# Optimization experiments

Hardware: AMD Instinct MI355X
Metric: run time of the kernel (lower is better)

Reference implementation:

```python
import jax, jax.numpy as jnp
import numpy as np

_LOG_2PI = float(np.log(2.0 * np.pi))
N = 4096
N_VARS = 128
N_SOURCES = 8
_EPS = 1e-6


def setup_inputs() -> dict:
    key = jax.random.key(0)
    ks = jax.random.split(key, 6)
    data = jax.random.normal(ks[0], (N, N_VARS), dtype=jnp.float32)
    sources = jax.random.randint(ks[1], (N,), 0, N_SOURCES, dtype=jnp.int32)
    miss_mask = jax.random.bernoulli(ks[2], 0.3, (N, N_VARS))
    # Strictly lower-triangular DAG weights, small spectral norm so I - W is well conditioned
    W_eff = jnp.tril(jax.random.normal(ks[3], (N_VARS, N_VARS), dtype=jnp.float32) * 0.05, k=-1)
    log_sigma2 = jnp.zeros((N_SOURCES, N_VARS), dtype=jnp.float32)
    mu = jnp.zeros((N_VARS,), dtype=jnp.float32)
    sample_weights = jax.random.uniform(ks[4], (N,), dtype=jnp.float32)
    return {"data": data, "W_eff": W_eff, "log_sigma2": log_sigma2, "mu": mu,
            "sample_weights": sample_weights, "sources": sources, "miss_mask": miss_mask}


def reference(data, W_eff, log_sigma2, mu, sample_weights, sources, miss_mask):
    # Gaussian log-likelihood over observed entries only, per sample.
    # Original torch code loops over unique (source, missingness-pattern) groups and
    # does a Cholesky of the observed sub-covariance Sigma_oo + eps*I.  We compute the
    # mathematically identical quantity fully batched via the masked-covariance trick:
    #   Sigma_tilde = M (Sigma + eps I) M + diag(1 - obs)
    # whose logdet equals logdet(Sigma_oo + eps I_oo) and whose quadratic form on the
    # zero-filled centred data equals x_o^T (Sigma_oo + eps I)^{-1} x_o.
    D = data.shape[1]
    I = jnp.eye(D, dtype=data.dtype)
    T = jnp.linalg.solve(I - W_eff, I)                       # [D, D]
    sigma2 = jnp.maximum(jnp.exp(log_sigma2), _EPS)          # [S, D]
    # Sigma_s = T^T diag(sigma2_s) T for every source
    Sigma = jnp.einsum('ij,si,ik->sjk', T, sigma2, T)        # [S, D, D]

    obs = (~miss_mask).astype(data.dtype)                    # [N, D]
    xc = (data - mu[None, :]) * obs                          # centred, zero at missing

    Sig_i = Sigma[sources] + _EPS * I                        # [N, D, D]
    M = obs[:, :, None] * obs[:, None, :]                    # [N, D, D] obs outer obs
    Sig_t = Sig_i * M + I * (1.0 - obs)[:, None, :]          # identity on missing coords

    L = jnp.linalg.cholesky(Sig_t)                           # [N, D, D]
    z = jax.scipy.linalg.solve_triangular(L, xc[:, :, None], lower=True)[:, :, 0]
    quad = jnp.sum(z * z, axis=1)                            # [N]
    logdet = 2.0 * jnp.sum(jnp.log(jnp.diagonal(L, axis1=1, axis2=2)), axis=1)
    d_obs = jnp.sum(obs, axis=1)                             # [N]
    ll = -0.5 * (quad + logdet + d_obs * _LOG_2PI)           # [N]
    return jnp.sum(ll * sample_weights)
```

## Files before the change

### kernel.cpp

```cpp
#include <hip/hip_runtime.h>
#include <math.h>

#define DD 128
#define NSRC 8
#define EMAX 32
#define MFAST 62
#define LOG_2PI 1.83787706640934548356f
#define LN2F 0.69314718055994531f
#define EPSF 1e-6f

__device__ inline int tri_row_of(int e) {
    float f = sqrtf(8.f * (float)e + 1.f);
    int r = (int)((f - 1.f) * 0.5f);
    if ((r + 1) * (r + 2) / 2 <= e) ++r;
    else if (r * (r + 1) / 2 > e) --r;
    return r;
}

__global__ __launch_bounds__(128) void k_precompute(
    const float* __restrict__ W, const float* __restrict__ ls2,
    const unsigned int* __restrict__ mw, int n_words,
    float* __restrict__ Q, float* __restrict__ ldS,
    int* __restrict__ flagarr, float* __restrict__ partial,
    int* __restrict__ ovf_cnt)
{
    __shared__ float Bs[DD][DD + 1];
    __shared__ float r[4][DD + 1];
    __shared__ float sinv[DD];
    __shared__ float part2[2];
    __shared__ int fsh[2];
    const int tid = threadIdx.x;
    const int s   = blockIdx.x >> 5;
    const int i0  = (blockIdx.x & 31) * 4;

    if (blockIdx.x == 0) {
        if (tid < 64)  partial[tid] = 0.f;
        if (tid == 64) *ovf_cnt = 0;
    }

    int gid = (blockIdx.x * 128 + tid) * 4;
    int f = 0;
    #pragma unroll
    for (int t = 0; t < 4; ++t) {
        int idx = gid + t;
        if (idx < n_words) {
            unsigned int v = mw[idx];
            if (v > 1u) f |= 1;
            if (v == 0x3F800000u) f |= 2;
        }
    }
    unsigned long long bA = __ballot(f & 1);
    unsigned long long bB = __ballot(f & 2);
    if ((tid & 63) == 0) fsh[tid >> 6] = (bA ? 1 : 0) | (bB ? 2 : 0);

    for (int idx = tid; idx < DD * DD; idx += 128) {
        int row = idx >> 7, col = idx & 127;
        Bs[row][col] = (row == col ? 1.f : 0.f) - W[idx];
    }
    sinv[tid] = 1.f / fmaxf(expf(ls2[s * DD + tid]), EPSF);
    __syncthreads();
    if (tid == 0) flagarr[blockIdx.x] = fsh[0] | fsh[1];
    for (int a = 0; a < 4; ++a)
        r[a][tid] = Bs[i0 + a][tid] * sinv[tid];
    __syncthreads();

    const int j = tid;
    float acc0 = 0.f, acc1 = 0.f, acc2 = 0.f, acc3 = 0.f;
    #pragma unroll 4
    for (int d = 0; d < DD; ++d) {
        float bj = Bs[j][d];
        acc0 += r[0][d] * bj;
        acc1 += r[1][d] * bj;
        acc2 += r[2][d] * bj;
        acc3 += r[3][d] * bj;
    }
    size_t base = ((size_t)s * DD + i0) * DD + j;
    Q[base         ] = acc0;
    Q[base +     DD] = acc1;
    Q[base + 2 * DD] = acc2;
    Q[base + 3 * DD] = acc3;

    if (i0 == 0) {
        float v = logf(fmaxf(expf(ls2[s * DD + tid]), EPSF));
        for (int o = 32; o; o >>= 1) v += __shfl_down(v, o, 64);
        if ((tid & 63) == 0) part2[tid >> 6] = v;
        __syncthreads();
        if (tid == 0) ldS[s] = part2[0] + part2[1];
    }
}

__global__ __launch_bounds__(64) void k_fast(
    const float* __restrict__ data, const float* __restrict__ mu,
    const float* __restrict__ wgt, const int* __restrict__ src,
    const void* __restrict__ miss, const int* __restrict__ flagarr,
    const float* __restrict__ Q, const float* __restrict__ ldS,
    float* __restrict__ partial, int* __restrict__ ovf_cnt,
    int* __restrict__ ovf_list)
{
    __shared__ float xsh[DD];
    __shared__ float ysh[DD];
    __shared__ int   midx[64];
    __shared__ float csc[2][64];

    const int i = blockIdx.x, lane = threadIdx.x;
    const int s = src[i];
    const float* Qs = Q + (size_t)s * DD * DD;
    const size_t base = (size_t)i * DD;
    const int j0 = 2 * lane, j1 = 2 * lane + 1;

    int fl = 0;
    #pragma unroll
    for (int t = 0; t < 4; ++t) fl |= flagarr[lane + 64 * t];
    unsigned long long fb1 = __ballot(fl & 1);
    unsigned long long fb2 = __ballot(fl & 2);
    const int f = (fb1 ? 1 : 0) | (fb2 ? 2 : 0);

    bool mmE, mmO;
    if (f & 2) {
        const float* M = (const float*)miss;
        mmE = M[base + j0] != 0.f;  mmO = M[base + j1] != 0.f;
    } else if (f & 1) {
        const unsigned char* M = (const unsigned char*)miss;
        mmE = M[base + j0] != 0;    mmO = M[base + j1] != 0;
    } else {
        const int* M = (const int*)miss;
        mmE = M[base + j0] != 0;    mmO = M[base + j1] != 0;
    }

    unsigned long long bE = __ballot(mmE), bO = __ballot(mmO);
    const int m = __popcll(bE) + __popcll(bO);
    if (m > MFAST) {
        if (lane == 0) { int pos = atomicAdd(ovf_cnt, 1); ovf_list[pos] = i; }
        return;
    }
    unsigned long long lt = (1ull << lane) - 1ull;
    if (mmE) midx[__popcll(bE & lt)] = j0;
    if (mmO) midx[__popcll(bE) + __popcll(bO & lt)] = j1;

    float x0 = mmE ? 0.f : (data[base + j0] - mu[j0]);
    float x1 = mmO ? 0.f : (data[base + j1] - mu[j1]);
    xsh[j0] = x0;
    xsh[j1] = x1;
    __syncthreads();

    float y0 = 0.f, y1 = 0.f, z0 = 0.f, z1 = 0.f;
    #pragma unroll 8
    for (int k = 0; k < DD; k += 2) {
        float xk0 = xsh[k], xk1 = xsh[k + 1];
        float2 qa = *(const float2*)(Qs + (size_t)k * DD + j0);
        float2 qb = *(const float2*)(Qs + (size_t)(k + 1) * DD + j0);
        y0 += xk0 * qa.x;  y1 += xk0 * qa.y;
        z0 += xk1 * qb.x;  z1 += xk1 * qb.y;
    }
    y0 += z0;  y1 += z1;
    ysh[j0] = y0;
    ysh[j1] = y1;
    float p = x0 * y0 + x1 * y1;
    for (int o = 32; o; o >>= 1) p += __shfl_down(p, o, 64);
    __syncthreads();

    const int cntT = ((m + 1) * (m + 2)) >> 1;
    unsigned key[EMAX];
    float    val[EMAX];
    #pragma unroll
    for (int t = 0; t < EMAX; ++t) {
        key[t] = 0u; val[t] = 0.f;
        int e = lane + (t << 6);
        if (e < cntT) {
            int q  = tri_row_of(e);
            int jc = m - q;
            int ir = jc + (e - ((q * (q + 1)) >> 1));
            float v;
            if (ir == m) {
                v = (jc == m) ? 0.f : ysh[midx[jc]];
            } else {
                v = Qs[(size_t)(midx[ir] * DD + midx[jc])];
            }
            key[t] = ((unsigned)jc << 8) | (unsigned)ir;
            val[t] = v;
            if (jc == 0) csc[0][ir] = v;
        }
    }
    __syncthreads();

    float logacc = 0.f;
    #pragma unroll 1
    for (int k = 0; k < m; ++k) {
        const int pb = k & 1;
        float dk = csc[pb][k];
        float invd = __builtin_amdgcn_rcpf(dk);
        logacc += __log2f(dk);
        const unsigned boundA = (unsigned)(k + 1) << 8;
        const unsigned boundB = (unsigned)(k + 2) << 8;
        #pragma unroll
        for (int t = 0; t < EMAX; ++t) {
            bool alive = (key[t] >= boundA);
            if (!__any(alive)) break;
            if (alive) {
                int ir = (int)(key[t] & 255u);
                int jc = (int)(key[t] >> 8);
                float ci = csc[pb][ir];
                float cj = csc[pb][jc];
                val[t] -= ci * cj * invd;
                if (key[t] < boundB) csc[pb ^ 1][ir] = val[t];
            }
        }
        __syncthreads();
    }

    if (lane == 0) {
        float ll = -0.5f * ((p + val[0]) + logacc * LN2F + ldS[s]
                            + (float)(DD - m) * LOG_2PI);
        atomicAdd(&partial[i & 63], ll * wgt[i]);
    }
}

__global__ __launch_bounds__(128) void k_tail(
    const float* __restrict__ data, const float* __restrict__ mu,
    const float* __restrict__ wgt, const int* __restrict__ src,
    const void* __restrict__ miss, const int* __restrict__ flagarr,
    const float* __restrict__ Q, const float* __restrict__ ldS,
    float* __restrict__ partial, const int* __restrict__ ovf_cnt,
    const int* __restrict__ ovf_list, float* __restrict__ out)
{
    __shared__ __align__(16) float xsh[DD];
    __shared__ float ysh[DD];
    __shared__ int   midx[DD];
    __shared__ float cscv[DD + 1];
    __shared__ float tri[(DD + 1) * (DD + 2) / 2];
    __shared__ float bc[2];
    __shared__ float red[2];
    __shared__ int   sh_m;
    __shared__ int   sh_f;

    const int tid = threadIdx.x;
    if (tid == 0) sh_f = 0;
    __syncthreads();
    {
        int fl = flagarr[tid] | flagarr[tid + 128];
        if (fl) atomicOr(&sh_f, fl);
    }
    __syncthreads();
    const int f = sh_f;

    const int novf = *ovf_cnt;
    for (int j = 0; j < novf; ++j) {
        const int i = ovf_list[j];
        if (tid == 0) sh_m = 0;
        __syncthreads();

        const int s = src[i];
        const float* Qs = Q + (size_t)s * DD * DD;
        const size_t g = (size_t)i * DD + tid;
        bool mm;
        if (f & 2)      mm = ((const float*)miss)[g] != 0.f;
        else if (f & 1) mm = ((const unsigned char*)miss)[g] != 0;
        else            mm = ((const int*)miss)[g] != 0;

        float xv = mm ? 0.f : (data[g] - mu[tid]);
        xsh[tid] = xv;
        if (mm) { int pos = atomicAdd(&sh_m, 1); midx[pos] = tid; }
        __syncthreads();
        const int m = sh_m;

        const float4* qrow = (const float4*)(Qs + (size_t)tid * DD);
        const float4* x4   = (const float4*)xsh;
        float acc = 0.f;
        #pragma unroll 8
        for (int d = 0; d < DD / 4; ++d) {
            float4 q = qrow[d], xx = x4[d];
            acc += q.x * xx.x + q.y * xx.y + q.z * xx.z + q.w * xx.w;
        }
        ysh[tid] = acc;
        float pp = xv * acc;
        for (int o = 32; o; o >>= 1) pp += __shfl_down(pp, o, 64);
        if ((tid & 63) == 0) red[tid >> 6] = pp;
        __syncthreads();

        const int cntA = (m * (m + 1)) >> 1;
        for (int e = tid; e < cntA; e += 128) {
            int a = tri_row_of(e);
            int b = e - ((a * (a + 1)) >> 1);
            tri[e] = Qs[(size_t)midx[a] * DD + midx[b]];
        }
        for (int b = tid; b < m; b += 128) tri[cntA + b] = ysh[midx[b]];
        if (tid == 0) tri[cntA + m] = 0.f;
        __syncthreads();

        float logacc = 0.f;
        if (m > 0) {
            if (tid == 0) {
                float d0 = tri[0];
                bc[1] = d0;
                float sq = sqrtf(d0);
                bc[0] = 1.f / sq;
                tri[0] = sq;
            }
            __syncthreads();
            for (int k = 0; k < m; ++k) {
                float inv = bc[0];
                if (tid == 0) logacc += logf(bc[1]);
                for (int ii = k + 1 + tid; ii <= m; ii += 128) {
                    int off = (ii * (ii + 1)) >> 1;
                    float v = tri[off + k] * inv;
                    tri[off + k] = v;
                    cscv[ii] = v;
                }
                __syncthreads();
                int qn  = m - k;
                int cnt = (qn * (qn + 1)) >> 1;
                for (int e = tid; e < cnt; e += 128) {
                    int ri = tri_row_of(e);
                    int rj = e - ((ri * (ri + 1)) >> 1);
                    int ii = k + 1 + ri, jj = k + 1 + rj;
                    int off = (ii * (ii + 1)) >> 1;
                    float v = tri[off + jj] - cscv[ii] * cscv[jj];
                    if (ii == jj && jj == k + 1 && k + 1 < m) {
                        bc[1] = v;
                        float sq = sqrtf(v);
                        bc[0] = 1.f / sq;
                        tri[off + jj] = sq;
                    } else {
                        tri[off + jj] = v;
                    }
                }
                __syncthreads();
            }
        }

        if (tid == 0) {
            float quad2 = (m > 0) ? -tri[cntA + m] : 0.f;
            float quad1 = red[0] + red[1];
            float ll = -0.5f * ((quad1 - quad2) + logacc + ldS[s]
                                + (float)(DD - m) * LOG_2PI);
            atomicAdd(&partial[i & 63], ll * wgt[i]);
        }
        __syncthreads();
    }

    __syncthreads();
    if (tid < 64) {
        float v = partial[tid];
        for (int o = 32; o; o >>= 1) v += __shfl_down(v, o, 64);
        if (tid == 0) out[0] = v;
    }
}

extern "C" void kernel_launch(void* const* d_in, const int* in_sizes, int n_in,
                              void* d_out, int out_size, void* d_ws, size_t ws_size,
                              hipStream_t stream)
{
    const float* data = (const float*)d_in[0];
    const float* W    = (const float*)d_in[1];
    const float* ls2  = (const float*)d_in[2];
    const float* mu   = (const float*)d_in[3];
    const float* wgt  = (const float*)d_in[4];
    const int*   src  = (const int*)d_in[5];
    const void*  miss = (const void*)d_in[6];
    float* out = (float*)d_out;

    float* Q        = (float*)d_ws;
    float* ldS      = Q + (size_t)NSRC * DD * DD;
    float* partial  = ldS + NSRC;
    int*   flagarr  = (int*)(partial + 64);
    int*   ovf_cnt  = flagarr + 256;
    int*   ovf_list = ovf_cnt + 1;

    const int n       = in_sizes[0] / DD;
    const int n_words = (n * DD) / 4;

    hipLaunchKernelGGL(k_precompute, dim3(NSRC * 32), dim3(128), 0, stream,
                       W, ls2, (const unsigned int*)miss, n_words,
                       Q, ldS, flagarr, partial, ovf_cnt);
    hipLaunchKernelGGL(k_fast, dim3(n), dim3(64), 0, stream,
                       data, mu, wgt, src, miss, flagarr, Q, ldS,
                       partial, ovf_cnt, ovf_list);
    hipLaunchKernelGGL(k_tail, dim3(1), dim3(128), 0, stream,
                       data, mu, wgt, src, miss, flagarr, Q, ldS,
                       partial, ovf_cnt, ovf_list, out);
}
```

Baseline: 154.1 us.

## Process two samples per wavefront in k_fast to interleave independent eliminations

```diff
diff --git a/kernel.cpp b/kernel.cpp
--- a/kernel.cpp
+++ b/kernel.cpp
@@ -89,23 +89,28 @@
     }
 }
 
-__global__ __launch_bounds__(64) void k_fast(
+__global__ __launch_bounds__(64, 2) void k_fast(
     const float* __restrict__ data, const float* __restrict__ mu,
     const float* __restrict__ wgt, const int* __restrict__ src,
     const void* __restrict__ miss, const int* __restrict__ flagarr,
     const float* __restrict__ Q, const float* __restrict__ ldS,
     float* __restrict__ partial, int* __restrict__ ovf_cnt,
-    int* __restrict__ ovf_list)
+    int* __restrict__ ovf_list, int n)
 {
-    __shared__ float xsh[DD];
-    __shared__ float ysh[DD];
-    __shared__ int   midx[64];
-    __shared__ float csc[2][64];
-
-    const int i = blockIdx.x, lane = threadIdx.x;
-    const int s = src[i];
-    const float* Qs = Q + (size_t)s * DD * DD;
-    const size_t base = (size_t)i * DD;
+    __shared__ float xshA[DD], xshB[DD];
+    __shared__ float yshA[DD], yshB[DD];
+    __shared__ int   midxA[64], midxB[64];
+    __shared__ float cscA[2][64], cscB[2][64];
+
+    const int lane = threadIdx.x;
+    const int iA = blockIdx.x * 2;
+    const bool validB = (iA + 1) < n;
+    const int iB = validB ? (iA + 1) : iA;
+    const int sA = src[iA], sB = src[iB];
+    const float* QA = Q + (size_t)sA * DD * DD;
+    const float* QB = Q + (size_t)sB * DD * DD;
+    const size_t baseA = (size_t)iA * DD;
+    const size_t baseB = (size_t)iB * DD;
     const int j0 = 2 * lane, j1 = 2 * lane + 1;
 
     int fl = 0;
@@ -115,103 +120,163 @@
     unsigned long long fb2 = __ballot(fl & 2);
     const int f = (fb1 ? 1 : 0) | (fb2 ? 2 : 0);
 
-    bool mmE, mmO;
+    bool mAe, mAo, mBe, mBo;
     if (f & 2) {
         const float* M = (const float*)miss;
-        mmE = M[base + j0] != 0.f;  mmO = M[base + j1] != 0.f;
+        mAe = M[baseA + j0] != 0.f;  mAo = M[baseA + j1] != 0.f;
+        mBe = M[baseB + j0] != 0.f;  mBo = M[baseB + j1] != 0.f;
     } else if (f & 1) {
         const unsigned char* M = (const unsigned char*)miss;
-        mmE = M[base + j0] != 0;    mmO = M[base + j1] != 0;
+        mAe = M[baseA + j0] != 0;    mAo = M[baseA + j1] != 0;
+        mBe = M[baseB + j0] != 0;    mBo = M[baseB + j1] != 0;
     } else {
         const int* M = (const int*)miss;
-        mmE = M[base + j0] != 0;    mmO = M[base + j1] != 0;
-    }
-
-    unsigned long long bE = __ballot(mmE), bO = __ballot(mmO);
-    const int m = __popcll(bE) + __popcll(bO);
-    if (m > MFAST) {
-        if (lane == 0) { int pos = atomicAdd(ovf_cnt, 1); ovf_list[pos] = i; }
-        return;
-    }
+        mAe = M[baseA + j0] != 0;    mAo = M[baseA + j1] != 0;
+        mBe = M[baseB + j0] != 0;    mBo = M[baseB + j1] != 0;
+    }
+
+    unsigned long long bAE = __ballot(mAe), bAO = __ballot(mAo);
+    unsigned long long bBE = __ballot(mBe), bBO = __ballot(mBo);
+    const int mAr = __popcll(bAE) + __popcll(bAO);
+    const int mBr = __popcll(bBE) + __popcll(bBO);
+    const bool skipA = (mAr > MFAST);
+    const bool skipB = (mBr > MFAST) || !validB;
+    if (lane == 0) {
+        if (skipA)                    { int pos = atomicAdd(ovf_cnt, 1); ovf_list[pos] = iA; }
+        if (validB && (mBr > MFAST))  { int pos = atomicAdd(ovf_cnt, 1); ovf_list[pos] = iB; }
+    }
+    const int mA = skipA ? 0 : mAr;
+    const int mB = skipB ? 0 : mBr;
     unsigned long long lt = (1ull << lane) - 1ull;
-    if (mmE) midx[__popcll(bE & lt)] = j0;
-    if (mmO) midx[__popcll(bE) + __popcll(bO & lt)] = j1;
-
-    float x0 = mmE ? 0.f : (data[base + j0] - mu[j0]);
-    float x1 = mmO ? 0.f : (data[base + j1] - mu[j1]);
-    xsh[j0] = x0;
-    xsh[j1] = x1;
-    __syncthreads();
-
-    float y0 = 0.f, y1 = 0.f, z0 = 0.f, z1 = 0.f;
-    #pragma unroll 8
+    if (!skipA) {
+        if (mAe) midxA[__popcll(bAE & lt)] = j0;
+        if (mAo) midxA[__popcll(bAE) + __popcll(bAO & lt)] = j1;
+    }
+    if (!skipB) {
+        if (mBe) midxB[__popcll(bBE & lt)] = j0;
+        if (mBo) midxB[__popcll(bBE) + __popcll(bBO & lt)] = j1;
+    }
+
+    float xA0 = mAe ? 0.f : (data[baseA + j0] - mu[j0]);
+    float xA1 = mAo ? 0.f : (data[baseA + j1] - mu[j1]);
+    float xB0 = mBe ? 0.f : (data[baseB + j0] - mu[j0]);
+    float xB1 = mBo ? 0.f : (data[baseB + j1] - mu[j1]);
+    xshA[j0] = xA0;  xshA[j1] = xA1;
+    xshB[j0] = xB0;  xshB[j1] = xB1;
+    __syncthreads();
+
+    float yA0 = 0.f, yA1 = 0.f, zA0 = 0.f, zA1 = 0.f;
+    float yB0 = 0.f, yB1 = 0.f, zB0 = 0.f, zB1 = 0.f;
+    #pragma unroll 4
     for (int k = 0; k < DD; k += 2) {
-        float xk0 = xsh[k], xk1 = xsh[k + 1];
-        float2 qa = *(const float2*)(Qs + (size_t)k * DD + j0);
-        float2 qb = *(const float2*)(Qs + (size_t)(k + 1) * DD + j0);
-        y0 += xk0 * qa.x;  y1 += xk0 * qa.y;
-        z0 += xk1 * qb.x;  z1 += xk1 * qb.y;
-    }
-    y0 += z0;  y1 += z1;
-    ysh[j0] = y0;
-    ysh[j1] = y1;
-    float p = x0 * y0 + x1 * y1;
-    for (int o = 32; o; o >>= 1) p += __shfl_down(p, o, 64);
-    __syncthreads();
-
-    const int cntT = ((m + 1) * (m + 2)) >> 1;
-    unsigned key[EMAX];
-    float    val[EMAX];
+        float xkA0 = xshA[k], xkA1 = xshA[k + 1];
+        float xkB0 = xshB[k], xkB1 = xshB[k + 1];
+        float2 qa = *(const float2*)(QA + (size_t)k * DD + j0);
+        float2 qb = *(const float2*)(QA + (size_t)(k + 1) * DD + j0);
+        float2 qc = *(const float2*)(QB + (size_t)k * DD + j0);
+        float2 qd = *(const float2*)(QB + (size_t)(k + 1) * DD + j0);
+        yA0 += xkA0 * qa.x;  yA1 += xkA0 * qa.y;
+        zA0 += xkA1 * qb.x;  zA1 += xkA1 * qb.y;
+        yB0 += xkB0 * qc.x;  yB1 += xkB0 * qc.y;
+        zB0 += xkB1 * qd.x;  zB1 += xkB1 * qd.y;
+    }
+    yA0 += zA0;  yA1 += zA1;  yB0 += zB0;  yB1 += zB1;
+    yshA[j0] = yA0;  yshA[j1] = yA1;
+    yshB[j0] = yB0;  yshB[j1] = yB1;
+    float pA = xA0 * yA0 + xA1 * yA1;
+    float pB = xB0 * yB0 + xB1 * yB1;
+    for (int o = 32; o; o >>= 1) {
+        pA += __shfl_down(pA, o, 64);
+        pB += __shfl_down(pB, o, 64);
+    }
+    __syncthreads();
+
+    const int cntTA = ((mA + 1) * (mA + 2)) >> 1;
+    const int cntTB = ((mB + 1) * (mB + 2)) >> 1;
+    const int cntMax = cntTA > cntTB ? cntTA : cntTB;
+    unsigned keyA[EMAX], keyB[EMAX];
+    float    valA[EMAX], valB[EMAX];
     #pragma unroll
     for (int t = 0; t < EMAX; ++t) {
-        key[t] = 0u; val[t] = 0.f;
+        keyA[t] = 0u; valA[t] = 0.f;
+        keyB[t] = 0u; valB[t] = 0.f;
         int e = lane + (t << 6);
-        if (e < cntT) {
+        if (e < cntMax) {
             int q  = tri_row_of(e);
-            int jc = m - q;
-            int ir = jc + (e - ((q * (q + 1)) >> 1));
-            float v;
-            if (ir == m) {
-                v = (jc == m) ? 0.f : ysh[midx[jc]];
-            } else {
-                v = Qs[(size_t)(midx[ir] * DD + midx[jc])];
-            }
-            key[t] = ((unsigned)jc << 8) | (unsigned)ir;
-            val[t] = v;
-            if (jc == 0) csc[0][ir] = v;
-        }
-    }
-    __syncthreads();
-
-    float logacc = 0.f;
+            int eq = e - ((q * (q + 1)) >> 1);
+            if (e < cntTA) {
+                int jc = mA - q;
+                int ir = jc + eq;
+                float v;
+                if (ir == mA) v = (jc == mA) ? 0.f : yshA[midxA[jc]];
+                else          v = QA[(size_t)(midxA[ir] * DD + midxA[jc])];
+                keyA[t] = ((unsigned)jc << 8) | (unsigned)ir;
+                valA[t] = v;
+                if (jc == 0) cscA[0][ir] = v;
+            }
+            if (e < cntTB) {
+                int jc = mB - q;
+                int ir = jc + eq;
+                float v;
+                if (ir == mB) v = (jc == mB) ? 0.f : yshB[midxB[jc]];
+                else          v = QB[(size_t)(midxB[ir] * DD + midxB[jc])];
+                keyB[t] = ((unsigned)jc << 8) | (unsigned)ir;
+                valB[t] = v;
+                if (jc == 0) cscB[0][ir] = v;
+            }
+        }
+    }
+    __syncthreads();
+
+    float logA = 0.f, logB = 0.f;
+    const int mMax = mA > mB ? mA : mB;
     #pragma unroll 1
-    for (int k = 0; k < m; ++k) {
+    for (int k = 0; k < mMax; ++k) {
         const int pb = k & 1;
-        float dk = csc[pb][k];
-        float invd = __builtin_amdgcn_rcpf(dk);
-        logacc += __log2f(dk);
-        const unsigned boundA = (unsigned)(k + 1) << 8;
-        const unsigned boundB = (unsigned)(k + 2) << 8;
+        float dkA = cscA[pb][k];
+        float dkB = cscB[pb][k];
+        float invdA = __builtin_amdgcn_rcpf(dkA);
+        float invdB = __builtin_amdgcn_rcpf(dkB);
+        if (k < mA) logA += __log2f(dkA);
+        if (k < mB) logB += __log2f(dkB);
+        const unsigned b1 = (unsigned)(k + 1) << 8;
+        const unsigned b2 = (unsigned)(k + 2) << 8;
         #pragma unroll
         for (int t = 0; t < EMAX; ++t) {
-            bool alive = (key[t] >= boundA);
-            if (!__any(alive)) break;
-            if (alive) {
-                int ir = (int)(key[t] & 255u);
-                int jc = (int)(key[t] >> 8);
-                float ci = csc[pb][ir];
-                float cj = csc[pb][jc];
-                val[t] -= ci * cj * invd;
-                if (key[t] < boundB) csc[pb ^ 1][ir] = val[t];
+            bool aA = (keyA[t] >= b1);
+            bool aB = (keyB[t] >= b1);
+            if (!__any(aA | aB)) break;
+            if (aA) {
+                int ir = (int)(keyA[t] & 255u);
+                int jc = (int)(keyA[t] >> 8);
+                float ci = cscA[pb][ir];
+                float cj = cscA[pb][jc];
+                valA[t] -= ci * cj * invdA;
+                if (keyA[t] < b2) cscA[pb ^ 1][ir] = valA[t];
+            }
+            if (aB) {
+                int ir = (int)(keyB[t] & 255u);
+                int jc = (int)(keyB[t] >> 8);
+                float ci = cscB[pb][ir];
+                float cj = cscB[pb][jc];
+                valB[t] -= ci * cj * invdB;
+                if (keyB[t] < b2) cscB[pb ^ 1][ir] = valB[t];
             }
         }
         __syncthreads();
     }
 
     if (lane == 0) {
-        float ll = -0.5f * ((p + val[0]) + logacc * LN2F + ldS[s]
-                            + (float)(DD - m) * LOG_2PI);
-        atomicAdd(&partial[i & 63], ll * wgt[i]);
+        if (!skipA) {
+            float llA = -0.5f * ((pA + valA[0]) + logA * LN2F + ldS[sA]
+                                 + (float)(DD - mA) * LOG_2PI);
+            atomicAdd(&partial[iA & 63], llA * wgt[iA]);
+        }
+        if (!skipB) {
+            float llB = -0.5f * ((pB + valB[0]) + logB * LN2F + ldS[sB]
+                                 + (float)(DD - mB) * LOG_2PI);
+            atomicAdd(&partial[iB & 63], llB * wgt[iB]);
+        }
     }
 }
 
@@ -372,9 +437,9 @@
     hipLaunchKernelGGL(k_precompute, dim3(NSRC * 32), dim3(128), 0, stream,
                        W, ls2, (const unsigned int*)miss, n_words,
                        Q, ldS, flagarr, partial, ovf_cnt);
-    hipLaunchKernelGGL(k_fast, dim3(n), dim3(64), 0, stream,
+    hipLaunchKernelGGL(k_fast, dim3((n + 1) / 2), dim3(64), 0, stream,
                        data, mu, wgt, src, miss, flagarr, Q, ldS,
-                       partial, ovf_cnt, ovf_list);
+                       partial, ovf_cnt, ovf_list, n);
     hipLaunchKernelGGL(k_tail, dim3(1), dim3(128), 0, stream,
                        data, mu, wgt, src, miss, flagarr, Q, ldS,
                        partial, ovf_cnt, ovf_list, out);
```

Measured after the change: 181.0 us. 17.4% more time.

## Fold overflow tail kernel into fast kernel via last-block-done counter

Applied to the files above, without the earlier changes.

```diff
diff --git a/kernel.cpp b/kernel.cpp
--- a/kernel.cpp
+++ b/kernel.cpp
@@ -12,8 +12,8 @@
 __device__ inline int tri_row_of(int e) {
     float f = sqrtf(8.f * (float)e + 1.f);
     int r = (int)((f - 1.f) * 0.5f);
-    if ((r + 1) * (r + 2) / 2 <= e) ++r;
-    else if (r * (r + 1) / 2 > e) --r;
+    r += (int)((r + 1) * (r + 2) / 2 <= e);
+    r -= (int)(r * (r + 1) / 2 > e);
     return r;
 }
 
@@ -22,7 +22,7 @@
     const unsigned int* __restrict__ mw, int n_words,
     float* __restrict__ Q, float* __restrict__ ldS,
     int* __restrict__ flagarr, float* __restrict__ partial,
-    int* __restrict__ ovf_cnt)
+    int* __restrict__ ovf_cnt, int* __restrict__ done_cnt)
 {
     __shared__ float Bs[DD][DD + 1];
     __shared__ float r[4][DD + 1];
@@ -36,6 +36,7 @@
     if (blockIdx.x == 0) {
         if (tid < 64)  partial[tid] = 0.f;
         if (tid == 64) *ovf_cnt = 0;
+        if (tid == 65) *done_cnt = 0;
     }
 
     int gid = (blockIdx.x * 128 + tid) * 4;
@@ -53,9 +54,16 @@
     unsigned long long bB = __ballot(f & 2);
     if ((tid & 63) == 0) fsh[tid >> 6] = (bA ? 1 : 0) | (bB ? 2 : 0);
 
-    for (int idx = tid; idx < DD * DD; idx += 128) {
-        int row = idx >> 7, col = idx & 127;
-        Bs[row][col] = (row == col ? 1.f : 0.f) - W[idx];
+    const float4* __restrict__ W4 = (const float4*)W;
+    #pragma unroll 8
+    for (int idx = tid; idx < (DD * DD) / 4; idx += 128) {
+        float4 w = W4[idx];
+        int row = idx >> 5;
+        int col = (idx & 31) << 2;
+        Bs[row][col + 0] = ((col + 0) == row ? 1.f : 0.f) - w.x;
+        Bs[row][col + 1] = ((col + 1) == row ? 1.f : 0.f) - w.y;
+        Bs[row][col + 2] = ((col + 2) == row ? 1.f : 0.f) - w.z;
+        Bs[row][col + 3] = ((col + 3) == row ? 1.f : 0.f) - w.w;
     }
     sinv[tid] = 1.f / fmaxf(expf(ls2[s * DD + tid]), EPSF);
     __syncthreads();
@@ -66,7 +74,7 @@
 
     const int j = tid;
     float acc0 = 0.f, acc1 = 0.f, acc2 = 0.f, acc3 = 0.f;
-    #pragma unroll 4
+    #pragma unroll 8
     for (int d = 0; d < DD; ++d) {
         float bj = Bs[j][d];
         acc0 += r[0][d] * bj;
@@ -95,12 +103,15 @@
     const void* __restrict__ miss, const int* __restrict__ flagarr,
     const float* __restrict__ Q, const float* __restrict__ ldS,
     float* __restrict__ partial, int* __restrict__ ovf_cnt,
-    int* __restrict__ ovf_list)
+    int* __restrict__ ovf_list, int* __restrict__ done_cnt,
+    float* __restrict__ g_tri, float* __restrict__ out)
 {
     __shared__ float xsh[DD];
     __shared__ float ysh[DD];
-    __shared__ int   midx[64];
+    __shared__ int   midx[DD];
     __shared__ float csc[2][64];
+    __shared__ float cscv[DD + 1];
+    __shared__ float bcsh[2];
 
     const int i = blockIdx.x, lane = threadIdx.x;
     const int s = src[i];
@@ -129,221 +140,203 @@
 
     unsigned long long bE = __ballot(mmE), bO = __ballot(mmO);
     const int m = __popcll(bE) + __popcll(bO);
-    if (m > MFAST) {
+    const bool ovf = (m > MFAST);
+    if (ovf) {
         if (lane == 0) { int pos = atomicAdd(ovf_cnt, 1); ovf_list[pos] = i; }
-        return;
-    }
-    unsigned long long lt = (1ull << lane) - 1ull;
-    if (mmE) midx[__popcll(bE & lt)] = j0;
-    if (mmO) midx[__popcll(bE) + __popcll(bO & lt)] = j1;
-
-    float x0 = mmE ? 0.f : (data[base + j0] - mu[j0]);
-    float x1 = mmO ? 0.f : (data[base + j1] - mu[j1]);
-    xsh[j0] = x0;
-    xsh[j1] = x1;
-    __syncthreads();
-
-    float y0 = 0.f, y1 = 0.f, z0 = 0.f, z1 = 0.f;
-    #pragma unroll 8
-    for (int k = 0; k < DD; k += 2) {
-        float xk0 = xsh[k], xk1 = xsh[k + 1];
-        float2 qa = *(const float2*)(Qs + (size_t)k * DD + j0);
-        float2 qb = *(const float2*)(Qs + (size_t)(k + 1) * DD + j0);
-        y0 += xk0 * qa.x;  y1 += xk0 * qa.y;
-        z0 += xk1 * qb.x;  z1 += xk1 * qb.y;
-    }
-    y0 += z0;  y1 += z1;
-    ysh[j0] = y0;
-    ysh[j1] = y1;
-    float p = x0 * y0 + x1 * y1;
-    for (int o = 32; o; o >>= 1) p += __shfl_down(p, o, 64);
-    __syncthreads();
-
-    const int cntT = ((m + 1) * (m + 2)) >> 1;
-    unsigned key[EMAX];
-    float    val[EMAX];
-    #pragma unroll
-    for (int t = 0; t < EMAX; ++t) {
-        key[t] = 0u; val[t] = 0.f;
-        int e = lane + (t << 6);
-        if (e < cntT) {
-            int q  = tri_row_of(e);
-            int jc = m - q;
-            int ir = jc + (e - ((q * (q + 1)) >> 1));
-            float v;
-            if (ir == m) {
-                v = (jc == m) ? 0.f : ysh[midx[jc]];
-            } else {
-                v = Qs[(size_t)(midx[ir] * DD + midx[jc])];
-            }
-            key[t] = ((unsigned)jc << 8) | (unsigned)ir;
-            val[t] = v;
-            if (jc == 0) csc[0][ir] = v;
-        }
-    }
-    __syncthreads();
-
-    float logacc = 0.f;
-    #pragma unroll 1
-    for (int k = 0; k < m; ++k) {
-        const int pb = k & 1;
-        float dk = csc[pb][k];
-        float invd = __builtin_amdgcn_rcpf(dk);
-        logacc += __log2f(dk);
-        const unsigned boundA = (unsigned)(k + 1) << 8;
-        const unsigned boundB = (unsigned)(k + 2) << 8;
+    } else {
+        unsigned long long lt = (1ull << lane) - 1ull;
+        if (mmE) midx[__popcll(bE & lt)] = j0;
+        if (mmO) midx[__popcll(bE) + __popcll(bO & lt)] = j1;
+
+        float x0 = mmE ? 0.f : (data[base + j0] - mu[j0]);
+        float x1 = mmO ? 0.f : (data[base + j1] - mu[j1]);
+        xsh[j0] = x0;
+        xsh[j1] = x1;
+        __syncthreads();
+
+        float y0 = 0.f, y1 = 0.f, z0 = 0.f, z1 = 0.f;
+        #pragma unroll 8
+        for (int k = 0; k < DD; k += 2) {
+            float xk0 = xsh[k], xk1 = xsh[k + 1];
+            float2 qa = *(const float2*)(Qs + (size_t)k * DD + j0);
+            float2 qb = *(const float2*)(Qs + (size_t)(k + 1) * DD + j0);
+            y0 += xk0 * qa.x;  y1 += xk0 * qa.y;
+            z0 += xk1 * qb.x;  z1 += xk1 * qb.y;
+        }
+        y0 += z0;  y1 += z1;
+        ysh[j0] = y0;
+        ysh[j1] = y1;
+        float p = x0 * y0 + x1 * y1;
+        for (int o = 32; o; o >>= 1) p += __shfl_down(p, o, 64);
+        __syncthreads();
+
+        const int cntT = ((m + 1) * (m + 2)) >> 1;
+        unsigned key[EMAX];
+        float    val[EMAX];
         #pragma unroll
         for (int t = 0; t < EMAX; ++t) {
-            bool alive = (key[t] >= boundA);
-            if (!__any(alive)) break;
-            if (alive) {
-                int ir = (int)(key[t] & 255u);
-                int jc = (int)(key[t] >> 8);
-                float ci = csc[pb][ir];
-                float cj = csc[pb][jc];
-                val[t] -= ci * cj * invd;
-                if (key[t] < boundB) csc[pb ^ 1][ir] = val[t];
+            int e = lane + (t << 6);
+            const bool inr = (e < cntT);
+            int ec = inr ? e : 0;
+            int q  = tri_row_of(ec);
+            int jc = m - q;
+            int ir = jc + (ec - ((q * (q + 1)) >> 1));
+            const bool isQ = inr && (ir < m);
+            const bool isY = inr && (ir == m) && (jc < m);
+            int mi = midx[ir];
+            int mj = midx[jc];
+            int qa = isQ ? (mi * DD + mj) : 0;
+            float qv = Qs[(size_t)qa];
+            int ya = isY ? mj : 0;
+            float yv = ysh[ya];
+            float v = isQ ? qv : (isY ? yv : 0.f);
+            key[t] = inr ? (((unsigned)jc << 8) | (unsigned)ir) : 0u;
+            val[t] = v;
+            if (inr && jc == 0) csc[0][ir] = v;
+        }
+        __syncthreads();
+
+        float logacc = 0.f;
+        #pragma unroll 1
+        for (int k = 0; k < m; ++k) {
+            const int pb = k & 1;
+            float dk = csc[pb][k];
+            float invd = __builtin_amdgcn_rcpf(dk);
+            logacc += __log2f(dk);
+            const unsigned boundA = (unsigned)(k + 1) << 8;
+            const unsigned boundB = (unsigned)(k + 2) << 8;
+            #pragma unroll
+            for (int t = 0; t < EMAX; ++t) {
+                bool alive = (key[t] >= boundA);
+                if (!__any(alive)) break;
+                if (alive) {
+                    int ir = (int)(key[t] & 255u);
+                    int jc = (int)(key[t] >> 8);
+                    float ci = csc[pb][ir];
+                    float cj = csc[pb][jc];
+                    val[t] -= ci * cj * invd;
+                    if (key[t] < boundB) csc[pb ^ 1][ir] = val[t];
+                }
             }
-        }
-        __syncthreads();
-    }
-
-    if (lane == 0) {
-        float ll = -0.5f * ((p + val[0]) + logacc * LN2F + ldS[s]
-                            + (float)(DD - m) * LOG_2PI);
-        atomicAdd(&partial[i & 63], ll * wgt[i]);
-    }
-}
-
-__global__ __launch_bounds__(128) void k_tail(
-    const float* __restrict__ data, const float* __restrict__ mu,
-    const float* __restrict__ wgt, const int* __restrict__ src,
-    const void* __restrict__ miss, const int* __restrict__ flagarr,
-    const float* __restrict__ Q, const float* __restrict__ ldS,
-    float* __restrict__ partial, const int* __restrict__ ovf_cnt,
-    const int* __restrict__ ovf_list, float* __restrict__ out)
-{
-    __shared__ __align__(16) float xsh[DD];
-    __shared__ float ysh[DD];
-    __shared__ int   midx[DD];
-    __shared__ float cscv[DD + 1];
-    __shared__ float tri[(DD + 1) * (DD + 2) / 2];
-    __shared__ float bc[2];
-    __shared__ float red[2];
-    __shared__ int   sh_m;
-    __shared__ int   sh_f;
-
-    const int tid = threadIdx.x;
-    if (tid == 0) sh_f = 0;
-    __syncthreads();
-    {
-        int fl = flagarr[tid] | flagarr[tid + 128];
-        if (fl) atomicOr(&sh_f, fl);
-    }
-    __syncthreads();
-    const int f = sh_f;
-
-    const int novf = *ovf_cnt;
+            __syncthreads();
+        }
+
+        if (lane == 0) {
+            float ll = -0.5f * ((p + val[0]) + logacc * LN2F + ldS[s]
+                                + (float)(DD - m) * LOG_2PI);
+            atomicAdd(&partial[i & 63], ll * wgt[i]);
+        }
+    }
+
+    __threadfence();
+    int done = 0;
+    if (lane == 0) done = atomicAdd(done_cnt, 1);
+    done = __shfl(done, 0, 64);
+    if (done != (int)gridDim.x - 1) return;
+    __threadfence();
+
+    const int novf = *(volatile int*)ovf_cnt;
     for (int j = 0; j < novf; ++j) {
-        const int i = ovf_list[j];
-        if (tid == 0) sh_m = 0;
-        __syncthreads();
-
-        const int s = src[i];
-        const float* Qs = Q + (size_t)s * DD * DD;
-        const size_t g = (size_t)i * DD + tid;
-        bool mm;
-        if (f & 2)      mm = ((const float*)miss)[g] != 0.f;
-        else if (f & 1) mm = ((const unsigned char*)miss)[g] != 0;
-        else            mm = ((const int*)miss)[g] != 0;
-
-        float xv = mm ? 0.f : (data[g] - mu[tid]);
-        xsh[tid] = xv;
-        if (mm) { int pos = atomicAdd(&sh_m, 1); midx[pos] = tid; }
-        __syncthreads();
-        const int m = sh_m;
-
-        const float4* qrow = (const float4*)(Qs + (size_t)tid * DD);
-        const float4* x4   = (const float4*)xsh;
-        float acc = 0.f;
-        #pragma unroll 8
-        for (int d = 0; d < DD / 4; ++d) {
-            float4 q = qrow[d], xx = x4[d];
-            acc += q.x * xx.x + q.y * xx.y + q.z * xx.z + q.w * xx.w;
-        }
-        ysh[tid] = acc;
-        float pp = xv * acc;
+        const int smp = ((volatile const int*)ovf_list)[j];
+        const int s2 = src[smp];
+        const float* Qs2 = Q + (size_t)s2 * DD * DD;
+        const size_t g0 = (size_t)smp * DD + lane;
+        const size_t g1 = g0 + 64;
+        bool mm0, mm1;
+        if (f & 2) {
+            mm0 = ((const float*)miss)[g0] != 0.f;
+            mm1 = ((const float*)miss)[g1] != 0.f;
+        } else if (f & 1) {
+            mm0 = ((const unsigned char*)miss)[g0] != 0;
+            mm1 = ((const unsigned char*)miss)[g1] != 0;
+        } else {
+            mm0 = ((const int*)miss)[g0] != 0;
+            mm1 = ((const int*)miss)[g1] != 0;
+        }
+        unsigned long long b0 = __ballot(mm0), b1 = __ballot(mm1);
+        const int mt = __popcll(b0) + __popcll(b1);
+        unsigned long long lt2 = (1ull << lane) - 1ull;
+        if (mm0) midx[__popcll(b0 & lt2)] = lane;
+        if (mm1) midx[__popcll(b0) + __popcll(b1 & lt2)] = lane + 64;
+        float xv0 = mm0 ? 0.f : (data[g0] - mu[lane]);
+        float xv1 = mm1 ? 0.f : (data[g1] - mu[lane + 64]);
+        xsh[lane] = xv0;  xsh[lane + 64] = xv1;
+        __syncthreads();
+
+        float a0 = 0.f, a1 = 0.f;
+        for (int d = 0; d < DD; ++d) {
+            float xd = xsh[d];
+            a0 += Qs2[(size_t)lane * DD + d] * xd;
+            a1 += Qs2[(size_t)(lane + 64) * DD + d] * xd;
+        }
+        ysh[lane] = a0;  ysh[lane + 64] = a1;
+        float pp = xv0 * a0 + xv1 * a1;
         for (int o = 32; o; o >>= 1) pp += __shfl_down(pp, o, 64);
-        if ((tid & 63) == 0) red[tid >> 6] = pp;
-        __syncthreads();
-
-        const int cntA = (m * (m + 1)) >> 1;
-        for (int e = tid; e < cntA; e += 128) {
+        __syncthreads();
+
+        const int cntA = (mt * (mt + 1)) >> 1;
+        for (int e = lane; e < cntA; e += 64) {
             int a = tri_row_of(e);
             int b = e - ((a * (a + 1)) >> 1);
-            tri[e] = Qs[(size_t)midx[a] * DD + midx[b]];
-        }
-        for (int b = tid; b < m; b += 128) tri[cntA + b] = ysh[midx[b]];
-        if (tid == 0) tri[cntA + m] = 0.f;
-        __syncthreads();
-
-        float logacc = 0.f;
-        if (m > 0) {
-            if (tid == 0) {
-                float d0 = tri[0];
-                bc[1] = d0;
+            g_tri[e] = Qs2[(size_t)midx[a] * DD + midx[b]];
+        }
+        for (int b = lane; b < mt; b += 64) g_tri[cntA + b] = ysh[midx[b]];
+        if (lane == 0) g_tri[cntA + mt] = 0.f;
+        __syncthreads();
+
+        float logacc2 = 0.f;
+        if (mt > 0) {
+            if (lane == 0) {
+                float d0 = g_tri[0];
+                bcsh[1] = d0;
                 float sq = sqrtf(d0);
-                bc[0] = 1.f / sq;
-                tri[0] = sq;
+                bcsh[0] = 1.f / sq;
+                g_tri[0] = sq;
             }
             __syncthreads();
-            for (int k = 0; k < m; ++k) {
-                float inv = bc[0];
-                if (tid == 0) logacc += logf(bc[1]);
-                for (int ii = k + 1 + tid; ii <= m; ii += 128) {
-                    int off = (ii * (ii + 1)) >> 1;
-                    float v = tri[off + k] * inv;
-                    tri[off + k] = v;
-                    cscv[ii] = v;
+            for (int k = 0; k < mt; ++k) {
+                float inv = bcsh[0];
+                if (lane == 0) logacc2 += logf(bcsh[1]);
+                for (int r2 = k + 1 + lane; r2 <= mt; r2 += 64) {
+                    int off = (r2 * (r2 + 1)) >> 1;
+                    float vv = g_tri[off + k] * inv;
+                    g_tri[off + k] = vv;
+                    cscv[r2] = vv;
                 }
                 __syncthreads();
-                int qn  = m - k;
+                int qn  = mt - k;
                 int cnt = (qn * (qn + 1)) >> 1;
-                for (int e = tid; e < cnt; e += 128) {
+                for (int e = lane; e < cnt; e += 64) {
                     int ri = tri_row_of(e);
                     int rj = e - ((ri * (ri + 1)) >> 1);
-                    int ii = k + 1 + ri, jj = k + 1 + rj;
-                    int off = (ii * (ii + 1)) >> 1;
-                    float v = tri[off + jj] - cscv[ii] * cscv[jj];
-                    if (ii == jj && jj == k + 1 && k + 1 < m) {
-                        bc[1] = v;
-                        float sq = sqrtf(v);
-                        bc[0] = 1.f / sq;
-                        tri[off + jj] = sq;
+                    int i2 = k + 1 + ri, j2 = k + 1 + rj;
+                    int off = (i2 * (i2 + 1)) >> 1;
+                    float vv = g_tri[off + j2] - cscv[i2] * cscv[j2];
+                    if (i2 == j2 && j2 == k + 1 && k + 1 < mt) {
+                        bcsh[1] = vv;
+                        float sq = sqrtf(vv);
+                        bcsh[0] = 1.f / sq;
+                        g_tri[off + j2] = sq;
                     } else {
-                        tri[off + jj] = v;
+                        g_tri[off + j2] = vv;
                     }
                 }
                 __syncthreads();
             }
         }
 
-        if (tid == 0) {
-            float quad2 = (m > 0) ? -tri[cntA + m] : 0.f;
-            float quad1 = red[0] + red[1];
-            float ll = -0.5f * ((quad1 - quad2) + logacc + ldS[s]
-                                + (float)(DD - m) * LOG_2PI);
-            atomicAdd(&partial[i & 63], ll * wgt[i]);
-        }
-        __syncthreads();
-    }
-
-    __syncthreads();
-    if (tid < 64) {
-        float v = partial[tid];
-        for (int o = 32; o; o >>= 1) v += __shfl_down(v, o, 64);
-        if (tid == 0) out[0] = v;
-    }
+        if (lane == 0) {
+            float quad2 = (mt > 0) ? -g_tri[cntA + mt] : 0.f;
+            float ll = -0.5f * ((pp - quad2) + logacc2 + ldS[s2]
+                                + (float)(DD - mt) * LOG_2PI);
+            atomicAdd(&partial[smp & 63], ll * wgt[smp]);
+        }
+        __syncthreads();
+    }
+
+    float v = ((volatile float*)partial)[lane];
+    for (int o = 32; o; o >>= 1) v += __shfl_down(v, o, 64);
+    if (lane == 0) out[0] = v;
 }
 
 extern "C" void kernel_launch(void* const* d_in, const int* in_sizes, int n_in,
@@ -365,17 +358,16 @@
     int*   flagarr  = (int*)(partial + 64);
     int*   ovf_cnt  = flagarr + 256;
     int*   ovf_list = ovf_cnt + 1;
+    int*   done_cnt = ovf_list + 4096;
+    float* g_tri    = (float*)(done_cnt + 1);
 
     const int n       = in_sizes[0] / DD;
     const int n_words = (n * DD) / 4;
 
     hipLaunchKernelGGL(k_precompute, dim3(NSRC * 32), dim3(128), 0, stream,
                        W, ls2, (const unsigned int*)miss, n_words,
-                       Q, ldS, flagarr, partial, ovf_cnt);
+                       Q, ldS, flagarr, partial, ovf_cnt, done_cnt);
     hipLaunchKernelGGL(k_fast, dim3(n), dim3(64), 0, stream,
                        data, mu, wgt, src, miss, flagarr, Q, ldS,
-                       partial, ovf_cnt, ovf_list);
-    hipLaunchKernelGGL(k_tail, dim3(1), dim3(128), 0, stream,
-                       data, mu, wgt, src, miss, flagarr, Q, ldS,
-                       partial, ovf_cnt, ovf_list, out);
+                       partial, ovf_cnt, ovf_list, done_cnt, g_tri, out);
 }
```

New measurement: 218.6 us. 41.8% more time.

## Pack four samples per block in k_fast and vectorize W load in precompute

Applied to the files above, without the earlier changes.

```diff
diff --git a/kernel.cpp b/kernel.cpp
--- a/kernel.cpp
+++ b/kernel.cpp
@@ -5,6 +5,7 @@
 #define NSRC 8
 #define EMAX 32
 #define MFAST 62
+#define WPB 4
 #define LOG_2PI 1.83787706640934548356f
 #define LN2F 0.69314718055994531f
 #define EPSF 1e-6f
@@ -53,9 +54,16 @@
     unsigned long long bB = __ballot(f & 2);
     if ((tid & 63) == 0) fsh[tid >> 6] = (bA ? 1 : 0) | (bB ? 2 : 0);
 
-    for (int idx = tid; idx < DD * DD; idx += 128) {
-        int row = idx >> 7, col = idx & 127;
-        Bs[row][col] = (row == col ? 1.f : 0.f) - W[idx];
+    const float4* __restrict__ W4 = (const float4*)W;
+    #pragma unroll 8
+    for (int idx = tid; idx < (DD * DD) / 4; idx += 128) {
+        float4 w = W4[idx];
+        int row = idx >> 5;
+        int col = (idx & 31) << 2;
+        Bs[row][col + 0] = ((col + 0) == row ? 1.f : 0.f) - w.x;
+        Bs[row][col + 1] = ((col + 1) == row ? 1.f : 0.f) - w.y;
+        Bs[row][col + 2] = ((col + 2) == row ? 1.f : 0.f) - w.z;
+        Bs[row][col + 3] = ((col + 3) == row ? 1.f : 0.f) - w.w;
     }
     sinv[tid] = 1.f / fmaxf(expf(ls2[s * DD + tid]), EPSF);
     __syncthreads();
@@ -66,7 +74,7 @@
 
     const int j = tid;
     float acc0 = 0.f, acc1 = 0.f, acc2 = 0.f, acc3 = 0.f;
-    #pragma unroll 4
+    #pragma unroll 8
     for (int d = 0; d < DD; ++d) {
         float bj = Bs[j][d];
         acc0 += r[0][d] * bj;
@@ -89,24 +97,33 @@
     }
 }
 
-__global__ __launch_bounds__(64) void k_fast(
+__global__ __launch_bounds__(256) void k_fast(
     const float* __restrict__ data, const float* __restrict__ mu,
     const float* __restrict__ wgt, const int* __restrict__ src,
     const void* __restrict__ miss, const int* __restrict__ flagarr,
     const float* __restrict__ Q, const float* __restrict__ ldS,
     float* __restrict__ partial, int* __restrict__ ovf_cnt,
-    int* __restrict__ ovf_list)
+    int* __restrict__ ovf_list, int n)
 {
-    __shared__ float xsh[DD];
-    __shared__ float ysh[DD];
-    __shared__ int   midx[64];
-    __shared__ float csc[2][64];
-
-    const int i = blockIdx.x, lane = threadIdx.x;
+    __shared__ float xsh[WPB][DD];
+    __shared__ float ysh[WPB][DD];
+    __shared__ int   midx[WPB][64];
+    __shared__ float csc[WPB][2][64];
+
+    const int wv   = threadIdx.x >> 6;
+    const int lane = threadIdx.x & 63;
+    const int i    = blockIdx.x * WPB + wv;
+    if (i >= n) return;
+
     const int s = src[i];
     const float* Qs = Q + (size_t)s * DD * DD;
     const size_t base = (size_t)i * DD;
     const int j0 = 2 * lane, j1 = 2 * lane + 1;
+
+    float (* const xw)[DD]  = &xsh[wv];
+    float (* const yw)[DD]  = &ysh[wv];
+    int*   const mw_        = midx[wv];
+    float (* const cw)[64]  = csc[wv];
 
     int fl = 0;
     #pragma unroll
@@ -134,30 +151,30 @@
         return;
     }
     unsigned long long lt = (1ull << lane) - 1ull;
-    if (mmE) midx[__popcll(bE & lt)] = j0;
-    if (mmO) midx[__popcll(bE) + __popcll(bO & lt)] = j1;
+    if (mmE) mw_[__popcll(bE & lt)] = j0;
+    if (mmO) mw_[__popcll(bE) + __popcll(bO & lt)] = j1;
 
     float x0 = mmE ? 0.f : (data[base + j0] - mu[j0]);
     float x1 = mmO ? 0.f : (data[base + j1] - mu[j1]);
-    xsh[j0] = x0;
-    xsh[j1] = x1;
-    __syncthreads();
+    (*xw)[j0] = x0;
+    (*xw)[j1] = x1;
+    __threadfence_block();
 
     float y0 = 0.f, y1 = 0.f, z0 = 0.f, z1 = 0.f;
     #pragma unroll 8
     for (int k = 0; k < DD; k += 2) {
-        float xk0 = xsh[k], xk1 = xsh[k + 1];
+        float xk0 = (*xw)[k], xk1 = (*xw)[k + 1];
         float2 qa = *(const float2*)(Qs + (size_t)k * DD + j0);
         float2 qb = *(const float2*)(Qs + (size_t)(k + 1) * DD + j0);
         y0 += xk0 * qa.x;  y1 += xk0 * qa.y;
         z0 += xk1 * qb.x;  z1 += xk1 * qb.y;
     }
     y0 += z0;  y1 += z1;
-    ysh[j0] = y0;
-    ysh[j1] = y1;
+    (*yw)[j0] = y0;
+    (*yw)[j1] = y1;
     float p = x0 * y0 + x1 * y1;
     for (int o = 32; o; o >>= 1) p += __shfl_down(p, o, 64);
-    __syncthreads();
+    __threadfence_block();
 
     const int cntT = ((m + 1) * (m + 2)) >> 1;
     unsigned key[EMAX];
@@ -172,22 +189,22 @@
             int ir = jc + (e - ((q * (q + 1)) >> 1));
             float v;
             if (ir == m) {
-                v = (jc == m) ? 0.f : ysh[midx[jc]];
+                v = (jc == m) ? 0.f : (*yw)[mw_[jc]];
             } else {
-                v = Qs[(size_t)(midx[ir] * DD + midx[jc])];
+                v = Qs[(size_t)(mw_[ir] * DD + mw_[jc])];
             }
             key[t] = ((unsigned)jc << 8) | (unsigned)ir;
             val[t] = v;
-            if (jc == 0) csc[0][ir] = v;
-        }
-    }
-    __syncthreads();
+            if (jc == 0) cw[0][ir] = v;
+        }
+    }
+    __threadfence_block();
 
     float logacc = 0.f;
     #pragma unroll 1
     for (int k = 0; k < m; ++k) {
         const int pb = k & 1;
-        float dk = csc[pb][k];
+        float dk = cw[pb][k];
         float invd = __builtin_amdgcn_rcpf(dk);
         logacc += __log2f(dk);
         const unsigned boundA = (unsigned)(k + 1) << 8;
@@ -199,13 +216,13 @@
             if (alive) {
                 int ir = (int)(key[t] & 255u);
                 int jc = (int)(key[t] >> 8);
-                float ci = csc[pb][ir];
-                float cj = csc[pb][jc];
+                float ci = cw[pb][ir];
+                float cj = cw[pb][jc];
                 val[t] -= ci * cj * invd;
-                if (key[t] < boundB) csc[pb ^ 1][ir] = val[t];
+                if (key[t] < boundB) cw[pb ^ 1][ir] = val[t];
             }
         }
-        __syncthreads();
+        __threadfence_block();
     }
 
     if (lane == 0) {
@@ -372,9 +389,9 @@
     hipLaunchKernelGGL(k_precompute, dim3(NSRC * 32), dim3(128), 0, stream,
                        W, ls2, (const unsigned int*)miss, n_words,
                        Q, ldS, flagarr, partial, ovf_cnt);
-    hipLaunchKernelGGL(k_fast, dim3(n), dim3(64), 0, stream,
+    hipLaunchKernelGGL(k_fast, dim3((n + WPB - 1) / WPB), dim3(WPB * 64), 0, stream,
                        data, mu, wgt, src, miss, flagarr, Q, ldS,
-                       partial, ovf_cnt, ovf_list);
+                       partial, ovf_cnt, ovf_list, n);
     hipLaunchKernelGGL(k_tail, dim3(1), dim3(128), 0, stream,
                        data, mu, wgt, src, miss, flagarr, Q, ldS,
                        partial, ovf_cnt, ovf_list, out);
```

Result: slower. 162.5 us (+5.4%).
